# Optimization experiments

Measured on AMD Instinct MI355X. Metric: run time of the kernel, lower is better.

Reference implementation:

```python
import jax, jax.numpy as jnp
import numpy as np

NBX = 24  # nb_x_patches
NBY = 24  # nb_y_patches
B, H, D = 8, 12, 64
L = NBX * NBY + 1  # 577 (grid tokens + 1 CLS token from the pad)
EPS = 1e-08


def _toeplitz_mask(topological_params):
    # topological_params: [H, 4*NBX*NBY]
    gi = jnp.arange(NBX)
    gj = jnp.arange(NBY)
    # relative 2D displacement index, flattened over (i, j, i', j')
    dist_index = ((gi[:, None, None, None] - gi[None, None, :, None] + NBX) * 2 * NBY
                  + gj[None, :, None, None] - gj[None, None, None, :] + NBY)
    dist_index = dist_index.reshape(-1)
    m = jnp.take(topological_params, dist_index, axis=1)
    m = m.reshape(topological_params.shape[0], NBX * NBY, NBX * NBY)  # [H, L-1, L-1]
    # pad CLS row and column with 1.0
    m = jnp.pad(m, [[0, 0], [1, 0], [1, 0]], constant_values=1.0)  # [H, L, L]
    return m[None]  # [1, H, L, L]


def setup_inputs() -> dict:
    key = jax.random.key(0)
    k1, k2, k3, k4 = jax.random.split(key, 4)
    return {
        'query': jax.random.normal(k1, (B, L, H, D), dtype=jnp.float32),
        'key': jax.random.normal(k2, (B, L, H, D), dtype=jnp.float32),
        'value': jax.random.normal(k3, (B, L, H, D), dtype=jnp.float32),
        'topological_params': jax.random.normal(k4, (H, 4 * NBX * NBY), dtype=jnp.float32),
    }


def reference(query, key, value, topological_params):
    depth = query.shape[-1]
    q = query / jnp.sqrt(jnp.asarray(depth, query.dtype))
    # relu feature map (kernel_type == 'relu')
    q = jax.nn.relu(q) + EPS
    k = jax.nn.relu(key) + EPS
    attn = jnp.einsum('bqhd,bkhd->bhqk', q, k)  # [B, H, L, L]
    top_mask = _toeplitz_mask(topological_params)  # [1, H, L, L]
    attn = attn * jnp.abs(top_mask) + EPS
    attn = attn / jnp.sum(attn, axis=-1, keepdims=True)  # kernelized normalization (no softmax)
    return jnp.einsum('bhqk,bkhd->bqhd', attn, value)
```

## Files before the change

kernel.cpp:

```cpp
#include <hip/hip_runtime.h>


#define Lq 577
#define NH 12
#define NB 8
#define DD 64
#define PAR 2304
#define EPSf 1e-8f

#define VT_OFF 7090176ull
#define M2_OFF 14954496ull

#define KBLK 1731
#define VBLK 960
#define MBLK 480

typedef __attribute__((ext_vector_type(4))) float f32x4;
typedef __attribute__((ext_vector_type(8))) short s16x8;

__device__ __forceinline__ float bflo(unsigned int u) {
    return __builtin_bit_cast(float, u << 16);
}
__device__ __forceinline__ float bfhi(unsigned int u) {
    return __builtin_bit_cast(float, u & 0xffff0000u);
}
__device__ __forceinline__ unsigned int f2bf(float f) {
    unsigned int x = __builtin_bit_cast(unsigned int, f);
    return (x + 0x7fffu + ((x >> 16) & 1u)) >> 16;
}
__device__ __forceinline__ int imin(int a, int b) { return a < b ? a : b; }

__device__ __forceinline__ void gload_lds16(const unsigned short* g, unsigned short* l) {
    __builtin_amdgcn_global_load_lds(
        (const __attribute__((address_space(1))) unsigned int*)g,
        (__attribute__((address_space(3))) unsigned int*)l, 16, 0, 0);
}

__device__ __forceinline__ bool probe_f32(const void* Qg) {
    float x = fabsf(((const float*)Qg)[threadIdx.x]);
    unsigned long long hit = __ballot(x > 2.44140625e-4f && x < 64.0f);
    unsigned long long act = __ballot(1);
    return 2 * __popcll(hit) >= __popcll(act);
}

template <bool F32>
__device__ __forceinline__ void load8f(const void* G, size_t eidx, float* o) {
    if constexpr (F32) {
        const float* p = (const float*)G + eidx;
        float4 a = *(const float4*)p;
        float4 b = *(const float4*)(p + 4);
        o[0] = a.x; o[1] = a.y; o[2] = a.z; o[3] = a.w;
        o[4] = b.x; o[5] = b.y; o[6] = b.z; o[7] = b.w;
    } else {
        const unsigned short* p = (const unsigned short*)G + eidx;
        uint4 a = *(const uint4*)p;
        unsigned int u[4] = {a.x, a.y, a.z, a.w};
#pragma unroll
        for (int j = 0; j < 4; ++j) {
            o[2 * j]     = bflo(u[j]);
            o[2 * j + 1] = bfhi(u[j]);
        }
    }
}

template <bool F32>
__device__ void prep_k_body(const void* Kg, unsigned short* Kp, int bx) {
    size_t i8 = ((size_t)bx * 256 + threadIdx.x) * 8;
    float f[8];
    load8f<F32>(Kg, i8, f);
    unsigned int o[4];
#pragma unroll
    for (int j = 0; j < 4; ++j) {
        unsigned int lo = f2bf(fmaxf(f[2 * j], 0.0f) + EPSf);
        unsigned int hi = f2bf(fmaxf(f[2 * j + 1], 0.0f) + EPSf);
        o[j] = lo | (hi << 16);
    }
    *(uint4*)(Kp + i8) = make_uint4(o[0], o[1], o[2], o[3]);
}

template <bool F32>
__device__ void prep_vt_body(const void* Vg, unsigned short* Vt,
                             unsigned short* s, int id) {
    const int t  = threadIdx.x;
    const int kt = id % 10;
    const int h  = (id / 10) % NH;
    const int b  = id / 120;
    {
        int kl  = t >> 2;
        int dch = (t & 3) * 16;
        int k   = kt * 64 + kl;
        unsigned int pk[8] = {};
        if (k <= 576) {
            float f[16];
            size_t base = ((size_t)((b * Lq + k) * NH + h)) * DD + dch;
            load8f<F32>(Vg, base, f);
            load8f<F32>(Vg, base + 8, f + 8);
#pragma unroll
            for (int j = 0; j < 8; ++j) {
                float a0 = f[2 * j], a1 = f[2 * j + 1];
                a0 = (a0 == a0) ? a0 : 0.0f;
                a1 = (a1 == a1) ? a1 : 0.0f;
                pk[j] = f2bf(a0) | (f2bf(a1) << 16);
            }
        }
#pragma unroll
        for (int j = 0; j < 8; ++j)
            *(unsigned int*)&s[kl * 72 + dch + 2 * j] = pk[j];
    }
    __syncthreads();
    {
        int d   = t >> 2;
        int kch = (t & 3) * 16;
        unsigned int o[8];
#pragma unroll
        for (int j = 0; j < 8; ++j) {
            unsigned short v0 = s[(kch + 2 * j) * 72 + d];
            unsigned short v1 = s[(kch + 2 * j + 1) * 72 + d];
            o[j] = (unsigned int)v0 | ((unsigned int)v1 << 16);
        }
        size_t base = ((size_t)((b * NH + h) * 64 + d)) * 640 + kt * 64 + kch;
        *(uint4*)(Vt + base)     = make_uint4(o[0], o[1], o[2], o[3]);
        *(uint4*)(Vt + base + 8) = make_uint4(o[4], o[5], o[6], o[7]);
    }
}

template <bool F32>
__device__ void prep_m2_body(const void* Tg, unsigned short* M2, int id) {
    const int qg = id % 40;
    const int h  = id / 40;
    const int t    = threadIdx.x;
    const int cf   = t >> 6;
    const int lane = t & 63;
    const int lm   = lane & 15;
    const int g    = lane >> 4;
    const int q    = qg * 16 + lm;
    const bool qok = q < Lq;
    int cq = 0;
    if (qok && q > 0) {
        int qq = q - 1;
        int qi = (qq * 2731) >> 16;
        cq = qq + 24 * qi + 1176;
    }
    for (int kt = 0; kt < 10; ++kt) {
        unsigned int hv[4];
#pragma unroll
        for (int e = 0; e < 4; ++e) {
            int k = kt * 64 + cf * 16 + g * 4 + e;
            float m;
            if (!qok || k > 576) m = 0.0f;
            else if (k == 0 || q == 0) m = 1.0f;
            else {
                int kk = k - 1;
                int ki = (kk * 2731) >> 16;
                int idx = cq - (kk + 24 * ki);
                float pv = F32 ? ((const float*)Tg)[h * PAR + idx]
                               : bflo((unsigned int)((const unsigned short*)Tg)[h * PAR + idx]);
                m = fabsf(pv);
                m = (m == m) ? m : 0.0f;
            }
            hv[e] = f2bf(m);
        }
        size_t base = ((size_t)(((h * 40 + qg) * 10 + kt) * 4 + cf) * 64 + lane) * 4;
        *(uint2*)(M2 + base) = make_uint2(hv[0] | (hv[1] << 16), hv[2] | (hv[3] << 16));
    }
}

__global__ __launch_bounds__(256)
void prep_all(const void* __restrict__ Qg, const void* __restrict__ Kg,
              const void* __restrict__ Vg, const void* __restrict__ Tg,
              unsigned short* __restrict__ Kp, unsigned short* __restrict__ Vt,
              unsigned short* __restrict__ M2) {
    __shared__ unsigned short s[64 * 72];
    bool f32 = probe_f32(Qg);
    int bx = blockIdx.x;
    if (bx < KBLK) {
        if (f32) prep_k_body<true>(Kg, Kp, bx);
        else     prep_k_body<false>(Kg, Kp, bx);
    } else if (bx < KBLK + VBLK) {
        if (f32) prep_vt_body<true>(Vg, Vt, s, bx - KBLK);
        else     prep_vt_body<false>(Vg, Vt, s, bx - KBLK);
    } else {
        if (f32) prep_m2_body<true>(Tg, M2, bx - KBLK - VBLK);
        else     prep_m2_body<false>(Tg, M2, bx - KBLK - VBLK);
    }
}

template <bool F32>
__device__ void attn_body(const void* __restrict__ Qg,
                          const unsigned short* __restrict__ Kp,
                          const unsigned short* __restrict__ Vt,
                          const unsigned short* __restrict__ M2,
                          void* __restrict__ Og,
                          unsigned short* s_k, unsigned short* s_vt,
                          unsigned short* s_p) {
    const int tid  = threadIdx.x;
    const int w    = tid >> 6;
    const int lane = tid & 63;
    const int g    = lane >> 4;
    const int lm   = lane & 15;

    const int bid = blockIdx.x;
    const int qt  = bid / 96;
    const int bh  = bid - qt * 96;
    const int h   = bh % NH;
    const int b   = bh / NH;

    unsigned short* s_pw = s_p + w * 2048;

    const int q0w = qt * 64 + w * 32;

    s16x8 a_q[2][2];
#pragma unroll
    for (int s = 0; s < 2; ++s) {
        int qc = imin(q0w + s * 16 + lm, Lq - 1);
        size_t rbase = ((size_t)((b * Lq + qc) * NH + h)) * DD;
#pragma unroll
        for (int ds = 0; ds < 2; ++ds) {
            float f[8];
            load8f<F32>(Qg, rbase + ds * 32 + g * 8, f);
            s16x8 a;
#pragma unroll
            for (int j = 0; j < 8; ++j) {
                float v = fmaf(fmaxf(f[j], 0.0f), 0.125f, EPSf);
                a[j] = (short)f2bf(v);
            }
            a_q[s][ds] = a;
        }
    }

    const int r8 = lane >> 3;
    const int c8 = lane & 7;
    const int xr = (c8 ^ r8) * 8;
    const int x7 = lm & 7;

    const unsigned short* KpBH = Kp + (size_t)b * (Lq * NH * DD) + h * DD;
    const unsigned short* VtBH = Vt + (size_t)(b * NH + h) * 64 * 640;
    const unsigned short* Mw0  = M2 + (size_t)(h * 40 + qt * 4 + w * 2) * 10240 + lane * 4;
    const unsigned short* Mw1  = Mw0 + 10240;

    f32x4 o_acc[2][4] = {};
    float rs[2] = {};

    uint2 mcur[2][4], mnxt[2][4];

    auto stage = [&](int t, int buf) {
        int kbn = t * 64;
#pragma unroll
        for (int i = 0; i < 4; ++i) {
            int krow = imin(kbn + w * 32 + i * 8 + r8, Lq - 1);
            int drow = w * 32 + i * 8 + r8;
            unsigned short* kd = s_k  + buf * 4096 + (w * 32 + i * 8) * 64;
            unsigned short* vd = s_vt + buf * 4096 + (w * 32 + i * 8) * 64;
            gload_lds16(KpBH + (size_t)krow * (NH * DD) + xr, kd);
            gload_lds16(VtBH + (size_t)drow * 640 + kbn + xr, vd);
        }
    };

    stage(0, 0);
#pragma unroll
    for (int cf = 0; cf < 4; ++cf) {
        mcur[0][cf] = *(const uint2*)(Mw0 + cf * 256);
        mcur[1][cf] = *(const uint2*)(Mw1 + cf * 256);
    }

#pragma unroll 2
    for (int t = 0; t < 10; ++t) {
        const int cur = t & 1;
        __syncthreads();

        if (t < 9) {
            stage(t + 1, cur ^ 1);
#pragma unroll
            for (int cf = 0; cf < 4; ++cf) {
                mnxt[0][cf] = *(const uint2*)(Mw0 + (t + 1) * 1024 + cf * 256);
                mnxt[1][cf] = *(const uint2*)(Mw1 + (t + 1) * 1024 + cf * 256);
            }
        }

        const unsigned short* skb = s_k  + cur * 4096;
        const unsigned short* svb = s_vt + cur * 4096;

        f32x4 sf[2][4];
#pragma unroll
        for (int cf = 0; cf < 4; ++cf) {
            const unsigned short* skr = skb + (cf * 16 + lm) * 64;
            int co = (g ^ x7) * 8;
            s16x8 kf0 = *(const s16x8*)(skr + co);
            s16x8 kf1 = *(const s16x8*)(skr + (co ^ 32));
#pragma unroll
            for (int s = 0; s < 2; ++s) {
                f32x4 acc = {};
                acc = __builtin_amdgcn_mfma_f32_16x16x32_bf16(kf0, a_q[s][0], acc, 0, 0, 0);
                acc = __builtin_amdgcn_mfma_f32_16x16x32_bf16(kf1, a_q[s][1], acc, 0, 0, 0);
                sf[s][cf] = acc;
            }
        }

#pragma unroll
        for (int s = 0; s < 2; ++s)
#pragma unroll
            for (int cf = 0; cf < 4; ++cf) {
                float m0 = bflo(mcur[s][cf].x), m1 = bfhi(mcur[s][cf].x);
                float m2 = bflo(mcur[s][cf].y), m3 = bfhi(mcur[s][cf].y);
                float p0 = fmaf(fmaxf(sf[s][cf][0], 0.0f), m0, EPSf);
                float p1 = fmaf(fmaxf(sf[s][cf][1], 0.0f), m1, EPSf);
                float p2 = fmaf(fmaxf(sf[s][cf][2], 0.0f), m2, EPSf);
                float p3 = fmaf(fmaxf(sf[s][cf][3], 0.0f), m3, EPSf);
                rs[s] += (p0 + p1) + (p2 + p3);
                unsigned int d0 = f2bf(p0) | (f2bf(p1) << 16);
                unsigned int d1 = f2bf(p2) | (f2bf(p3) << 16);
                int col = ((cf * 2 + (g >> 1)) ^ x7) * 8 + (g & 1) * 4;
                *(uint2*)&s_pw[(s * 16 + lm) * 64 + col] = make_uint2(d0, d1);
            }

#pragma unroll
        for (int ks = 0; ks < 2; ++ks) {
            s16x8 pa[2];
#pragma unroll
            for (int s = 0; s < 2; ++s)
                pa[s] = *(const s16x8*)&s_pw[(s * 16 + lm) * 64 + ((ks * 4 + g) ^ x7) * 8];
#pragma unroll
            for (int df = 0; df < 4; ++df) {
                const unsigned short* svr = svb + (df * 16 + lm) * 64;
                s16x8 vb = *(const s16x8*)(svr + ((ks * 4 + g) ^ x7) * 8);
                o_acc[0][df] = __builtin_amdgcn_mfma_f32_16x16x32_bf16(pa[0], vb, o_acc[0][df], 0, 0, 0);
                o_acc[1][df] = __builtin_amdgcn_mfma_f32_16x16x32_bf16(pa[1], vb, o_acc[1][df], 0, 0, 0);
            }
        }

#pragma unroll
        for (int s = 0; s < 2; ++s)
#pragma unroll
            for (int cf = 0; cf < 4; ++cf) mcur[s][cf] = mnxt[s][cf];
    }

#pragma unroll
    for (int s = 0; s < 2; ++s) {
        float tot = rs[s];
        tot += __shfl_xor(tot, 16, 64);
        tot += __shfl_xor(tot, 32, 64);
        float inv = (tot > 0.0f) ? 1.0f / tot : 0.0f;
#pragma unroll
        for (int r = 0; r < 4; ++r) {
            int   qrow  = q0w + s * 16 + g * 4 + r;
            float inv_r = __shfl(inv, g * 4 + r, 64);
            if (qrow < Lq) {
                size_t base = ((size_t)((b * Lq + qrow) * NH + h)) * DD;
#pragma unroll
                for (int df = 0; df < 4; ++df) {
                    float val = o_acc[s][df][r] * inv_r;
                    if constexpr (F32)
                        ((float*)Og)[base + df * 16 + lm] = val;
                    else
                        ((unsigned short*)Og)[base + df * 16 + lm] = (unsigned short)f2bf(val);
                }
            }
        }
    }
}

__global__ __launch_bounds__(128, 2)
void fused_topo_attn(const void* __restrict__ Qg,
                     const unsigned short* __restrict__ Kp,
                     const unsigned short* __restrict__ Vt,
                     const unsigned short* __restrict__ M2,
                     void* __restrict__ Og) {
    __shared__ __align__(16) unsigned short s_k[2 * 64 * 64];
    __shared__ __align__(16) unsigned short s_vt[2 * 64 * 64];
    __shared__ __align__(16) unsigned short s_p[2 * 32 * 64];

    if (probe_f32(Qg)) attn_body<true>(Qg, Kp, Vt, M2, Og, s_k, s_vt, s_p);
    else               attn_body<false>(Qg, Kp, Vt, M2, Og, s_k, s_vt, s_p);
}

extern "C" void kernel_launch(void* const* d_in, const int* in_sizes, int n_in,
                              void* d_out, int out_size, void* d_ws, size_t ws_size,
                              hipStream_t stream) {
    (void)in_sizes; (void)n_in; (void)out_size; (void)ws_size;
    unsigned short* Kp = (unsigned short*)d_ws;
    unsigned short* Vt = (unsigned short*)((char*)d_ws + VT_OFF);
    unsigned short* M2 = (unsigned short*)((char*)d_ws + M2_OFF);

    prep_all<<<KBLK + VBLK + MBLK, 256, 0, stream>>>(
        d_in[0], d_in[1], d_in[2], d_in[3], Kp, Vt, M2);
    fused_topo_attn<<<960, 128, 0, stream>>>(d_in[0], Kp, Vt, M2, d_out);
}
```

Baseline: 123.6 us.

## Split key range across two wave pairs per block and reduce partials in LDS

Result: no change. 123.9 us (+0.3%).

```diff
diff --git a/kernel.cpp b/kernel.cpp
--- a/kernel.cpp
+++ b/kernel.cpp
@@ -198,6 +198,8 @@
     const int lane = tid & 63;
     const int g    = lane >> 4;
     const int lm   = lane & 15;
+    const int kh   = w >> 1;
+    const int wq   = w & 1;
 
     const int bid = blockIdx.x;
     const int qt  = bid / 96;
@@ -207,7 +209,7 @@
 
     unsigned short* s_pw = s_p + w * 2048;
 
-    const int q0w = qt * 64 + w * 32;
+    const int q0w = qt * 64 + wq * 32;
 
     s16x8 a_q[2][2];
 #pragma unroll
@@ -235,50 +237,40 @@
 
     const unsigned short* KpBH = Kp + (size_t)b * (Lq * NH * DD) + h * DD;
     const unsigned short* VtBH = Vt + (size_t)(b * NH + h) * 64 * 640;
-    const unsigned short* Mw0  = M2 + (size_t)(h * 40 + qt * 4 + w * 2) * 10240 + lane * 4;
+    const unsigned short* Mw0  = M2 + (size_t)(h * 40 + qt * 4 + wq * 2) * 10240 + lane * 4;
     const unsigned short* Mw1  = Mw0 + 10240;
 
     f32x4 o_acc[2][4] = {};
     float rs[2] = {};
 
-    uint2 mcur[2][4], mnxt[2][4];
-
-    auto stage = [&](int t, int buf) {
-        int kbn = t * 64;
-#pragma unroll
-        for (int i = 0; i < 4; ++i) {
-            int krow = imin(kbn + w * 32 + i * 8 + r8, Lq - 1);
-            int drow = w * 32 + i * 8 + r8;
-            unsigned short* kd = s_k  + buf * 4096 + (w * 32 + i * 8) * 64;
-            unsigned short* vd = s_vt + buf * 4096 + (w * 32 + i * 8) * 64;
-            gload_lds16(KpBH + (size_t)krow * (NH * DD) + xr, kd);
-            gload_lds16(VtBH + (size_t)drow * 640 + kbn + xr, vd);
-        }
-    };
-
-    stage(0, 0);
-#pragma unroll
-    for (int cf = 0; cf < 4; ++cf) {
-        mcur[0][cf] = *(const uint2*)(Mw0 + cf * 256);
-        mcur[1][cf] = *(const uint2*)(Mw1 + cf * 256);
-    }
-
-#pragma unroll 2
-    for (int t = 0; t < 10; ++t) {
-        const int cur = t & 1;
+    const int kb0 = kh * 320;
+    unsigned short* skb = s_k  + kh * 4096;
+    unsigned short* svb = s_vt + kh * 4096;
+
+#pragma unroll 1
+    for (int t = 0; t < 5; ++t) {
         __syncthreads();
 
-        if (t < 9) {
-            stage(t + 1, cur ^ 1);
+        {
+            int kbn = kb0 + t * 64;
+#pragma unroll
+            for (int i = 0; i < 4; ++i) {
+                int drow = wq * 32 + i * 8;
+                int krow = imin(kbn + drow + r8, Lq - 1);
+                gload_lds16(KpBH + (size_t)krow * (NH * DD) + xr, skb + drow * 64);
+                gload_lds16(VtBH + (size_t)(drow + r8) * 640 + kbn + xr, svb + drow * 64);
+            }
+        }
+        uint2 mu[2][4];
+        {
+            int mo = (kh * 5 + t) * 1024;
 #pragma unroll
             for (int cf = 0; cf < 4; ++cf) {
-                mnxt[0][cf] = *(const uint2*)(Mw0 + (t + 1) * 1024 + cf * 256);
-                mnxt[1][cf] = *(const uint2*)(Mw1 + (t + 1) * 1024 + cf * 256);
-            }
-        }
-
-        const unsigned short* skb = s_k  + cur * 4096;
-        const unsigned short* svb = s_vt + cur * 4096;
+                mu[0][cf] = *(const uint2*)(Mw0 + mo + cf * 256);
+                mu[1][cf] = *(const uint2*)(Mw1 + mo + cf * 256);
+            }
+        }
+        __syncthreads();
 
         f32x4 sf[2][4];
 #pragma unroll
@@ -300,8 +292,8 @@
         for (int s = 0; s < 2; ++s)
 #pragma unroll
             for (int cf = 0; cf < 4; ++cf) {
-                float m0 = bflo(mcur[s][cf].x), m1 = bfhi(mcur[s][cf].x);
-                float m2 = bflo(mcur[s][cf].y), m3 = bfhi(mcur[s][cf].y);
+                float m0 = bflo(mu[s][cf].x), m1 = bfhi(mu[s][cf].x);
+                float m2 = bflo(mu[s][cf].y), m3 = bfhi(mu[s][cf].y);
                 float p0 = fmaf(fmaxf(sf[s][cf][0], 0.0f), m0, EPSf);
                 float p1 = fmaf(fmaxf(sf[s][cf][1], 0.0f), m1, EPSf);
                 float p2 = fmaf(fmaxf(sf[s][cf][2], 0.0f), m2, EPSf);
@@ -327,39 +319,62 @@
                 o_acc[1][df] = __builtin_amdgcn_mfma_f32_16x16x32_bf16(pa[1], vb, o_acc[1][df], 0, 0, 0);
             }
         }
-
+    }
+
+    __syncthreads();
+    float* scr = (float*)s_k;
+    float* rsb = (float*)s_vt;
+
+    float tot[2];
+#pragma unroll
+    for (int s = 0; s < 2; ++s) {
+        float v = rs[s];
+        v += __shfl_xor(v, 16, 64);
+        v += __shfl_xor(v, 32, 64);
+        tot[s] = v;
+    }
+
+    if (kh == 1) {
+        rsb[(wq * 2 + 0) * 64 + lane] = tot[0];
+        rsb[(wq * 2 + 1) * 64 + lane] = tot[1];
 #pragma unroll
         for (int s = 0; s < 2; ++s)
 #pragma unroll
-            for (int cf = 0; cf < 4; ++cf) mcur[s][cf] = mnxt[s][cf];
-    }
-
-#pragma unroll
-    for (int s = 0; s < 2; ++s) {
-        float tot = rs[s];
-        tot += __shfl_xor(tot, 16, 64);
-        tot += __shfl_xor(tot, 32, 64);
-        float inv = (tot > 0.0f) ? 1.0f / tot : 0.0f;
-#pragma unroll
-        for (int r = 0; r < 4; ++r) {
-            int   qrow  = q0w + s * 16 + g * 4 + r;
-            float inv_r = __shfl(inv, g * 4 + r, 64);
-            if (qrow < Lq) {
-                size_t base = ((size_t)((b * Lq + qrow) * NH + h)) * DD;
-#pragma unroll
-                for (int df = 0; df < 4; ++df) {
-                    float val = o_acc[s][df][r] * inv_r;
-                    if constexpr (F32)
-                        ((float*)Og)[base + df * 16 + lm] = val;
-                    else
-                        ((unsigned short*)Og)[base + df * 16 + lm] = (unsigned short)f2bf(val);
+            for (int df = 0; df < 4; ++df)
+                *(f32x4*)&scr[wq * 2048 + (s * 4 + df) * 256 + lane * 4] = o_acc[s][df];
+    }
+    __syncthreads();
+    if (kh == 0) {
+#pragma unroll
+        for (int s = 0; s < 2; ++s) {
+            float gtot = tot[s] + rsb[(wq * 2 + s) * 64 + lane];
+            float inv  = (gtot > 0.0f) ? 1.0f / gtot : 0.0f;
+#pragma unroll
+            for (int df = 0; df < 4; ++df) {
+                f32x4 part = *(const f32x4*)&scr[wq * 2048 + (s * 4 + df) * 256 + lane * 4];
+                o_acc[s][df] += part;
+            }
+#pragma unroll
+            for (int r = 0; r < 4; ++r) {
+                int   qrow  = q0w + s * 16 + g * 4 + r;
+                float inv_r = __shfl(inv, g * 4 + r, 64);
+                if (qrow < Lq) {
+                    size_t base = ((size_t)((b * Lq + qrow) * NH + h)) * DD;
+#pragma unroll
+                    for (int df = 0; df < 4; ++df) {
+                        float val = o_acc[s][df][r] * inv_r;
+                        if constexpr (F32)
+                            ((float*)Og)[base + df * 16 + lm] = val;
+                        else
+                            ((unsigned short*)Og)[base + df * 16 + lm] = (unsigned short)f2bf(val);
+                    }
                 }
             }
         }
     }
 }
 
-__global__ __launch_bounds__(128, 2)
+__global__ __launch_bounds__(256, 3)
 void fused_topo_attn(const void* __restrict__ Qg,
                      const unsigned short* __restrict__ Kp,
                      const unsigned short* __restrict__ Vt,
@@ -367,7 +382,7 @@
                      void* __restrict__ Og) {
     __shared__ __align__(16) unsigned short s_k[2 * 64 * 64];
     __shared__ __align__(16) unsigned short s_vt[2 * 64 * 64];
-    __shared__ __align__(16) unsigned short s_p[2 * 32 * 64];
+    __shared__ __align__(16) unsigned short s_p[4 * 32 * 64];
 
     if (probe_f32(Qg)) attn_body<true>(Qg, Kp, Vt, M2, Og, s_k, s_vt, s_p);
     else               attn_body<false>(Qg, Kp, Vt, M2, Og, s_k, s_vt, s_p);
@@ -383,5 +398,5 @@
 
     prep_all<<<KBLK + VBLK + MBLK, 256, 0, stream>>>(
         d_in[0], d_in[1], d_in[2], d_in[3], Kp, Vt, M2);
-    fused_topo_attn<<<960, 128, 0, stream>>>(d_in[0], Kp, Vt, M2, d_out);
-}
+    fused_topo_attn<<<960, 256, 0, stream>>>(d_in[0], Kp, Vt, M2, d_out);
+}
```

## Process 128 query rows per block with single-buffered K/V tiles

Applied to the files above, without the earlier changes.

Result: slower. 137.8 us (+11.5%).

```diff
diff --git a/kernel.cpp b/kernel.cpp
--- a/kernel.cpp
+++ b/kernel.cpp
@@ -205,13 +205,13 @@
     const int h   = bh % NH;
     const int b   = bh / NH;
 
-    unsigned short* s_pw = s_p + w * 2048;
-
-    const int q0w = qt * 64 + w * 32;
-
-    s16x8 a_q[2][2];
-#pragma unroll
-    for (int s = 0; s < 2; ++s) {
+    unsigned short* s_pw = s_p + w * 4096;
+
+    const int q0w = qt * 128 + w * 64;
+
+    s16x8 a_q[4][2];
+#pragma unroll
+    for (int s = 0; s < 4; ++s) {
         int qc = imin(q0w + s * 16 + lm, Lq - 1);
         size_t rbase = ((size_t)((b * Lq + qc) * NH + h)) * DD;
 #pragma unroll
@@ -235,107 +235,87 @@
 
     const unsigned short* KpBH = Kp + (size_t)b * (Lq * NH * DD) + h * DD;
     const unsigned short* VtBH = Vt + (size_t)(b * NH + h) * 64 * 640;
-    const unsigned short* Mw0  = M2 + (size_t)(h * 40 + qt * 4 + w * 2) * 10240 + lane * 4;
-    const unsigned short* Mw1  = Mw0 + 10240;
-
-    f32x4 o_acc[2][4] = {};
-    float rs[2] = {};
-
-    uint2 mcur[2][4], mnxt[2][4];
-
-    auto stage = [&](int t, int buf) {
-        int kbn = t * 64;
-#pragma unroll
-        for (int i = 0; i < 4; ++i) {
-            int krow = imin(kbn + w * 32 + i * 8 + r8, Lq - 1);
-            int drow = w * 32 + i * 8 + r8;
-            unsigned short* kd = s_k  + buf * 4096 + (w * 32 + i * 8) * 64;
-            unsigned short* vd = s_vt + buf * 4096 + (w * 32 + i * 8) * 64;
-            gload_lds16(KpBH + (size_t)krow * (NH * DD) + xr, kd);
-            gload_lds16(VtBH + (size_t)drow * 640 + kbn + xr, vd);
-        }
-    };
-
-    stage(0, 0);
-#pragma unroll
-    for (int cf = 0; cf < 4; ++cf) {
-        mcur[0][cf] = *(const uint2*)(Mw0 + cf * 256);
-        mcur[1][cf] = *(const uint2*)(Mw1 + cf * 256);
-    }
-
-#pragma unroll 2
+    const unsigned short* MwB  = M2 + (size_t)(h * 40 + qt * 8 + w * 4) * 10240 + lane * 4;
+
+    f32x4 o_acc[4][4] = {};
+    float rs[4] = {};
+
+#pragma unroll 1
     for (int t = 0; t < 10; ++t) {
-        const int cur = t & 1;
         __syncthreads();
 
-        if (t < 9) {
-            stage(t + 1, cur ^ 1);
+        {
+            int kbn = t * 64;
+#pragma unroll
+            for (int i = 0; i < 4; ++i) {
+                int drow = w * 32 + i * 8;
+                int krow = imin(kbn + drow + r8, Lq - 1);
+                gload_lds16(KpBH + (size_t)krow * (NH * DD) + xr, s_k + drow * 64);
+                gload_lds16(VtBH + (size_t)(drow + r8) * 640 + kbn + xr, s_vt + drow * 64);
+            }
+        }
+        __syncthreads();
+
+        s16x8 kf[4][2];
+#pragma unroll
+        for (int cf = 0; cf < 4; ++cf) {
+            const unsigned short* skr = s_k + (cf * 16 + lm) * 64;
+            int co = (g ^ x7) * 8;
+            kf[cf][0] = *(const s16x8*)(skr + co);
+            kf[cf][1] = *(const s16x8*)(skr + (co ^ 32));
+        }
+
+#pragma unroll
+        for (int s = 0; s < 4; ++s) {
+            uint2 mu[4];
+#pragma unroll
+            for (int cf = 0; cf < 4; ++cf)
+                mu[cf] = *(const uint2*)(MwB + s * 10240 + t * 1024 + cf * 256);
+
+            f32x4 sf[4];
 #pragma unroll
             for (int cf = 0; cf < 4; ++cf) {
-                mnxt[0][cf] = *(const uint2*)(Mw0 + (t + 1) * 1024 + cf * 256);
-                mnxt[1][cf] = *(const uint2*)(Mw1 + (t + 1) * 1024 + cf * 256);
-            }
-        }
-
-        const unsigned short* skb = s_k  + cur * 4096;
-        const unsigned short* svb = s_vt + cur * 4096;
-
-        f32x4 sf[2][4];
-#pragma unroll
-        for (int cf = 0; cf < 4; ++cf) {
-            const unsigned short* skr = skb + (cf * 16 + lm) * 64;
-            int co = (g ^ x7) * 8;
-            s16x8 kf0 = *(const s16x8*)(skr + co);
-            s16x8 kf1 = *(const s16x8*)(skr + (co ^ 32));
-#pragma unroll
-            for (int s = 0; s < 2; ++s) {
                 f32x4 acc = {};
-                acc = __builtin_amdgcn_mfma_f32_16x16x32_bf16(kf0, a_q[s][0], acc, 0, 0, 0);
-                acc = __builtin_amdgcn_mfma_f32_16x16x32_bf16(kf1, a_q[s][1], acc, 0, 0, 0);
-                sf[s][cf] = acc;
-            }
-        }
-
-#pragma unroll
-        for (int s = 0; s < 2; ++s)
+                acc = __builtin_amdgcn_mfma_f32_16x16x32_bf16(kf[cf][0], a_q[s][0], acc, 0, 0, 0);
+                acc = __builtin_amdgcn_mfma_f32_16x16x32_bf16(kf[cf][1], a_q[s][1], acc, 0, 0, 0);
+                sf[cf] = acc;
+            }
 #pragma unroll
             for (int cf = 0; cf < 4; ++cf) {
-                float m0 = bflo(mcur[s][cf].x), m1 = bfhi(mcur[s][cf].x);
-                float m2 = bflo(mcur[s][cf].y), m3 = bfhi(mcur[s][cf].y);
-                float p0 = fmaf(fmaxf(sf[s][cf][0], 0.0f), m0, EPSf);
-                float p1 = fmaf(fmaxf(sf[s][cf][1], 0.0f), m1, EPSf);
-                float p2 = fmaf(fmaxf(sf[s][cf][2], 0.0f), m2, EPSf);
-                float p3 = fmaf(fmaxf(sf[s][cf][3], 0.0f), m3, EPSf);
+                float m0 = bflo(mu[cf].x), m1 = bfhi(mu[cf].x);
+                float m2 = bflo(mu[cf].y), m3 = bfhi(mu[cf].y);
+                float p0 = fmaf(fmaxf(sf[cf][0], 0.0f), m0, EPSf);
+                float p1 = fmaf(fmaxf(sf[cf][1], 0.0f), m1, EPSf);
+                float p2 = fmaf(fmaxf(sf[cf][2], 0.0f), m2, EPSf);
+                float p3 = fmaf(fmaxf(sf[cf][3], 0.0f), m3, EPSf);
                 rs[s] += (p0 + p1) + (p2 + p3);
                 unsigned int d0 = f2bf(p0) | (f2bf(p1) << 16);
                 unsigned int d1 = f2bf(p2) | (f2bf(p3) << 16);
                 int col = ((cf * 2 + (g >> 1)) ^ x7) * 8 + (g & 1) * 4;
                 *(uint2*)&s_pw[(s * 16 + lm) * 64 + col] = make_uint2(d0, d1);
             }
+        }
 
 #pragma unroll
         for (int ks = 0; ks < 2; ++ks) {
-            s16x8 pa[2];
-#pragma unroll
-            for (int s = 0; s < 2; ++s)
+            s16x8 pa[4];
+#pragma unroll
+            for (int s = 0; s < 4; ++s)
                 pa[s] = *(const s16x8*)&s_pw[(s * 16 + lm) * 64 + ((ks * 4 + g) ^ x7) * 8];
 #pragma unroll
             for (int df = 0; df < 4; ++df) {
-                const unsigned short* svr = svb + (df * 16 + lm) * 64;
+                const unsigned short* svr = s_vt + (df * 16 + lm) * 64;
                 s16x8 vb = *(const s16x8*)(svr + ((ks * 4 + g) ^ x7) * 8);
-                o_acc[0][df] = __builtin_amdgcn_mfma_f32_16x16x32_bf16(pa[0], vb, o_acc[0][df], 0, 0, 0);
-                o_acc[1][df] = __builtin_amdgcn_mfma_f32_16x16x32_bf16(pa[1], vb, o_acc[1][df], 0, 0, 0);
-            }
-        }
-
-#pragma unroll
-        for (int s = 0; s < 2; ++s)
-#pragma unroll
-            for (int cf = 0; cf < 4; ++cf) mcur[s][cf] = mnxt[s][cf];
-    }
-
-#pragma unroll
-    for (int s = 0; s < 2; ++s) {
+#pragma unroll
+                for (int s = 0; s < 4; ++s)
+                    o_acc[s][df] = __builtin_amdgcn_mfma_f32_16x16x32_bf16(pa[s], vb,
+                                                                           o_acc[s][df], 0, 0, 0);
+            }
+        }
+    }
+
+#pragma unroll
+    for (int s = 0; s < 4; ++s) {
         float tot = rs[s];
         tot += __shfl_xor(tot, 16, 64);
         tot += __shfl_xor(tot, 32, 64);
@@ -365,9 +345,9 @@
                      const unsigned short* __restrict__ Vt,
                      const unsigned short* __restrict__ M2,
                      void* __restrict__ Og) {
-    __shared__ __align__(16) unsigned short s_k[2 * 64 * 64];
-    __shared__ __align__(16) unsigned short s_vt[2 * 64 * 64];
-    __shared__ __align__(16) unsigned short s_p[2 * 32 * 64];
+    __shared__ __align__(16) unsigned short s_k[64 * 64];
+    __shared__ __align__(16) unsigned short s_vt[64 * 64];
+    __shared__ __align__(16) unsigned short s_p[2 * 64 * 64];
 
     if (probe_f32(Qg)) attn_body<true>(Qg, Kp, Vt, M2, Og, s_k, s_vt, s_p);
     else               attn_body<false>(Qg, Kp, Vt, M2, Og, s_k, s_vt, s_p);
@@ -383,5 +363,5 @@
 
     prep_all<<<KBLK + VBLK + MBLK, 256, 0, stream>>>(
         d_in[0], d_in[1], d_in[2], d_in[3], Kp, Vt, M2);
-    fused_topo_attn<<<960, 128, 0, stream>>>(d_in[0], Kp, Vt, M2, d_out);
-}
+    fused_topo_attn<<<480, 128, 0, stream>>>(d_in[0], Kp, Vt, M2, d_out);
+}
```
